# Performance work log

Measured on AMD Instinct MI355X. Metric: run time of the kernel, lower is better.

The kernel has to match this reference:

```python
import jax, jax.numpy as jnp
import numpy as np

BATCH = 16384
NUM_Q = 100000
NUM_TAGS = 1024
DIFF_FEAT = 3
DIM = 64
HIDDEN = 128


def setup_inputs() -> dict:
    key = jax.random.key(0)
    ks = jax.random.split(key, 10)
    questions = jax.random.randint(ks[0], (BATCH,), 0, NUM_Q, dtype=jnp.int64 if jax.config.jax_enable_x64 else jnp.int32)
    question_skill_targets = jax.random.randint(ks[1], (BATCH, NUM_TAGS), 0, 2, dtype=jnp.int32)
    difficulty_feats = jax.random.normal(ks[2], (BATCH, DIFF_FEAT), dtype=jnp.float32)
    Q_emb = jax.random.normal(ks[3], (NUM_Q, DIM), dtype=jnp.float32) * 0.02
    S_emb = jax.random.normal(ks[4], (NUM_TAGS, DIM), dtype=jnp.float32) * 0.02
    W_diff = jax.random.normal(ks[5], (DIFF_FEAT, DIM), dtype=jnp.float32) * 0.1
    b_diff = jnp.zeros((DIM,), dtype=jnp.float32)
    W_fc = jax.random.normal(ks[6], (3 * DIM + 3, HIDDEN), dtype=jnp.float32) * 0.05
    b_fc = jnp.zeros((HIDDEN,), dtype=jnp.float32)
    W_out = jax.random.normal(ks[7], (HIDDEN, 1), dtype=jnp.float32) * 0.05
    b_out = jnp.zeros((1,), dtype=jnp.float32)
    return {"questions": questions, "question_skill_targets": question_skill_targets,
            "difficulty_feats": difficulty_feats, "Q_emb": Q_emb, "S_emb": S_emb,
            "W_diff": W_diff, "b_diff": b_diff, "W_fc": W_fc, "b_fc": b_fc,
            "W_out": W_out, "b_out": b_out}


def reference(questions, question_skill_targets, difficulty_feats,
              Q_emb, S_emb, W_diff, b_diff, W_fc, b_fc, W_out, b_out):
    # Ragged segment-mean over skill sets: mean of skill embeddings whose
    # multi-hot entry is nonzero == (T @ S) / count per row.
    t = question_skill_targets.astype(jnp.float32)            # [B, T]
    counts = jnp.sum(t, axis=1, keepdims=True)                # [B, 1] (>=1 w.h.p.)
    mu_skill = (t @ S_emb) / counts                           # [B, D]
    q = Q_emb[questions]                                      # [B, D]
    a = difficulty_feats @ W_diff + b_diff                    # [B, D]
    # PNN product layer: pairwise inner products + concat linear signals
    p12 = jnp.sum(q * mu_skill, axis=-1, keepdims=True)
    p13 = jnp.sum(q * a, axis=-1, keepdims=True)
    p23 = jnp.sum(mu_skill * a, axis=-1, keepdims=True)
    z = jnp.concatenate([q, mu_skill, a, p12, p13, p23], axis=-1)  # [B, 3D+3]
    e = jax.nn.relu(z @ W_fc + b_fc)                          # [B, H]
    p = jax.nn.sigmoid(e @ W_out + b_out)[:, 0]               # [B]
    return (e, p)
```

## Files before the change

kernel.cpp:

```cpp
#include <hip/hip_runtime.h>
#include <hip/hip_bf16.h>

#define BATCH   16384
#define NTAGS   1024
#define DIM     64
#define HID     128

typedef __attribute__((ext_vector_type(8))) short bf16x8;
typedef __attribute__((ext_vector_type(4))) float f32x4;

__device__ __forceinline__ unsigned short f2bf(float v) {
    unsigned u = __builtin_bit_cast(unsigned, v);
    return (unsigned short)((u + 0x7FFFu + ((u >> 16) & 1u)) >> 16);
}
__device__ __forceinline__ float bf2f(unsigned short u) {
    return __builtin_bit_cast(float, ((unsigned)u) << 16);
}

__global__ __launch_bounds__(256) void prep_pack(const float* __restrict__ S,
                                                 const float* __restrict__ Wfc,
                                                 unsigned short* __restrict__ Spack,
                                                 unsigned short* __restrict__ Wp)
{
    int tid = blockIdx.x * 256 + threadIdx.x;
    if (tid < 65536) {
        int j = tid & 7, l = (tid >> 3) & 63, nf = (tid >> 9) & 3, ks = tid >> 11;
        int k = ks * 32 + (l >> 4) * 8 + j;
        int d = nf * 16 + (l & 15);
        Spack[tid] = f2bf(S[k * 64 + d]);
    } else if (tid < 65536 + 24576) {
        int t2 = tid - 65536;
        int j = t2 & 7, l = (t2 >> 3) & 63, ct = (t2 >> 9) & 7, kt = t2 >> 12;
        int k = kt * 32 + (l >> 4) * 8 + j;
        int col = ct * 16 + (l & 15);
        Wp[t2] = f2bf(Wfc[k * 128 + col]);
    }
}

__global__ __launch_bounds__(256) void mega_kernel(
    const int* __restrict__ questions, const int* __restrict__ T,
    const float* __restrict__ dfeat, const float* __restrict__ Qemb,
    const float* __restrict__ Wdiff, const float* __restrict__ bdiff,
    const float* __restrict__ Wfc, const float* __restrict__ bfc,
    const float* __restrict__ Wout, const float* __restrict__ bout,
    const unsigned short* __restrict__ Spack, const unsigned short* __restrict__ Wp,
    float* __restrict__ out_e, float* __restrict__ out_p)
{
    __shared__ alignas(16) unsigned short zb[4][16][200];
    __shared__ float cnt16[4][16];
    __shared__ float scal[4][16][3];

    const int tid  = threadIdx.x;
    const int lane = tid & 63;
    const int wid  = tid >> 6;
    const int g    = lane >> 4;
    const int rl   = lane & 15;
    const int wrow = (blockIdx.x * 4 + wid) * 16;

    unsigned short (*z)[200] = zb[wid];
    float* cw = cnt16[wid];
    float (*sc)[3] = scal[wid];

    f32x4 a0{}, a1{}, a2{}, a3{};
    int c = 0;
    {
        const int* tp = T + (size_t)(wrow + rl) * 1024 + g * 8;
        const unsigned short* sp = Spack + lane * 8;

        int4 t0 = *(const int4*)(tp);
        int4 t1 = *(const int4*)(tp + 4);
#pragma unroll
        for (int st = 0; st < 32; ++st) {
            int4 c0 = t0, c1 = t1;
            if (st < 31) {
                t0 = *(const int4*)(tp + (st + 1) * 32);
                t1 = *(const int4*)(tp + (st + 1) * 32 + 4);
            }
            c += c0.x + c0.y + c0.z + c0.w + c1.x + c1.y + c1.z + c1.w;
            bf16x8 af;
            af[0] = (short)((-c0.x) & 0x3F80);
            af[1] = (short)((-c0.y) & 0x3F80);
            af[2] = (short)((-c0.z) & 0x3F80);
            af[3] = (short)((-c0.w) & 0x3F80);
            af[4] = (short)((-c1.x) & 0x3F80);
            af[5] = (short)((-c1.y) & 0x3F80);
            af[6] = (short)((-c1.z) & 0x3F80);
            af[7] = (short)((-c1.w) & 0x3F80);

            const unsigned short* s2 = sp + st * 2048;
            bf16x8 b0 = *(const bf16x8*)(s2);
            bf16x8 b1 = *(const bf16x8*)(s2 + 512);
            bf16x8 b2 = *(const bf16x8*)(s2 + 1024);
            bf16x8 b3 = *(const bf16x8*)(s2 + 1536);

            a0 = __builtin_amdgcn_mfma_f32_16x16x32_bf16(af, b0, a0, 0, 0, 0);
            a1 = __builtin_amdgcn_mfma_f32_16x16x32_bf16(af, b1, a1, 0, 0, 0);
            a2 = __builtin_amdgcn_mfma_f32_16x16x32_bf16(af, b2, a2, 0, 0, 0);
            a3 = __builtin_amdgcn_mfma_f32_16x16x32_bf16(af, b3, a3, 0, 0, 0);
        }
    }
    c += __shfl_xor(c, 16);
    c += __shfl_xor(c, 32);
    if (lane < 16) cw[lane] = (float)c;

    {
        float inv[4];
#pragma unroll
        for (int r = 0; r < 4; ++r) inv[r] = 1.f / cw[g * 4 + r];
#pragma unroll
        for (int r = 0; r < 4; ++r) {
            int row = g * 4 + r;
            z[row][64 + rl]      = f2bf(a0[r] * inv[r]);
            z[row][64 + 16 + rl] = f2bf(a1[r] * inv[r]);
            z[row][64 + 32 + rl] = f2bf(a2[r] * inv[r]);
            z[row][64 + 48 + rl] = f2bf(a3[r] * inv[r]);
        }
    }

    {
        int r = lane >> 2, q4 = lane & 3, d0 = q4 * 16;
        int row = wrow + r;
        int qi = questions[row];

        float q[16], aa[16], mu[16];
#pragma unroll
        for (int b = 0; b < 4; ++b) {
            float4 v = *(const float4*)(Qemb + (size_t)qi * 64 + d0 + b * 4);
            q[b * 4 + 0] = v.x; q[b * 4 + 1] = v.y; q[b * 4 + 2] = v.z; q[b * 4 + 3] = v.w;
        }
        float f0 = dfeat[row * 3 + 0];
        float f1 = dfeat[row * 3 + 1];
        float f2 = dfeat[row * 3 + 2];
#pragma unroll
        for (int b = 0; b < 4; ++b) {
            float4 w0 = *(const float4*)(Wdiff + d0 + b * 4);
            float4 w1 = *(const float4*)(Wdiff + 64 + d0 + b * 4);
            float4 w2 = *(const float4*)(Wdiff + 128 + d0 + b * 4);
            float4 bd = *(const float4*)(bdiff + d0 + b * 4);
            aa[b * 4 + 0] = bd.x + f0 * w0.x + f1 * w1.x + f2 * w2.x;
            aa[b * 4 + 1] = bd.y + f0 * w0.y + f1 * w1.y + f2 * w2.y;
            aa[b * 4 + 2] = bd.z + f0 * w0.z + f1 * w1.z + f2 * w2.z;
            aa[b * 4 + 3] = bd.w + f0 * w0.w + f1 * w1.w + f2 * w2.w;
        }
#pragma unroll
        for (int b = 0; b < 2; ++b) {
            ushort4 m0 = *(const ushort4*)&z[r][64 + d0 + b * 8];
            ushort4 m1 = *(const ushort4*)&z[r][64 + d0 + b * 8 + 4];
            mu[b * 8 + 0] = bf2f(m0.x); mu[b * 8 + 1] = bf2f(m0.y);
            mu[b * 8 + 2] = bf2f(m0.z); mu[b * 8 + 3] = bf2f(m0.w);
            mu[b * 8 + 4] = bf2f(m1.x); mu[b * 8 + 5] = bf2f(m1.y);
            mu[b * 8 + 6] = bf2f(m1.z); mu[b * 8 + 7] = bf2f(m1.w);
        }
        float s12 = 0.f, s13 = 0.f, s23 = 0.f;
#pragma unroll
        for (int d = 0; d < 16; ++d) {
            s12 += q[d] * mu[d];
            s13 += q[d] * aa[d];
            s23 += mu[d] * aa[d];
        }
        s12 += __shfl_xor(s12, 1); s12 += __shfl_xor(s12, 2);
        s13 += __shfl_xor(s13, 1); s13 += __shfl_xor(s13, 2);
        s23 += __shfl_xor(s23, 1); s23 += __shfl_xor(s23, 2);
        if (q4 == 0) { sc[r][0] = s12; sc[r][1] = s13; sc[r][2] = s23; }

        ushort4 v;
#pragma unroll
        for (int b = 0; b < 4; ++b) {
            v.x = f2bf(q[b * 4 + 0]); v.y = f2bf(q[b * 4 + 1]);
            v.z = f2bf(q[b * 4 + 2]); v.w = f2bf(q[b * 4 + 3]);
            *(ushort4*)&z[r][d0 + b * 4] = v;
        }
#pragma unroll
        for (int b = 0; b < 4; ++b) {
            v.x = f2bf(aa[b * 4 + 0]); v.y = f2bf(aa[b * 4 + 1]);
            v.z = f2bf(aa[b * 4 + 2]); v.w = f2bf(aa[b * 4 + 3]);
            *(ushort4*)&z[r][128 + d0 + b * 4] = v;
        }
    }

    {
        bf16x8 afr[6];
#pragma unroll
        for (int kt = 0; kt < 6; ++kt)
            afr[kt] = *(const bf16x8*)&z[rl][kt * 32 + g * 8];

        float s0 = sc[g * 4 + 0][0], s1 = sc[g * 4 + 0][1], s2 = sc[g * 4 + 0][2];
        float t0_ = sc[g * 4 + 1][0], t1_ = sc[g * 4 + 1][1], t2_ = sc[g * 4 + 1][2];
        float u0 = sc[g * 4 + 2][0], u1 = sc[g * 4 + 2][1], u2 = sc[g * 4 + 2][2];
        float v0 = sc[g * 4 + 3][0], v1 = sc[g * 4 + 3][1], v2 = sc[g * 4 + 3][2];

        float pr0 = 0.f, pr1 = 0.f, pr2 = 0.f, pr3 = 0.f;
#pragma unroll
        for (int ct = 0; ct < 8; ++ct) {
            f32x4 e{};
            const unsigned short* wp = Wp + (size_t)ct * 512 + lane * 8;
#pragma unroll
            for (int kt = 0; kt < 6; ++kt) {
                bf16x8 bfr = *(const bf16x8*)(wp + (size_t)kt * 4096);
                e = __builtin_amdgcn_mfma_f32_16x16x32_bf16(afr[kt], bfr, e, 0, 0, 0);
            }
            int h = ct * 16 + rl;
            float w192 = Wfc[192 * 128 + h];
            float w193 = Wfc[193 * 128 + h];
            float w194 = Wfc[194 * 128 + h];
            float bb = bfc[h];
            float wo = Wout[h];

            float ev;
            ev = e[0] + bb + s0 * w192 + s1 * w193 + s2 * w194;
            ev = ev > 0.f ? ev : 0.f;
            out_e[(size_t)(wrow + g * 4 + 0) * 128 + h] = ev;  pr0 += ev * wo;
            ev = e[1] + bb + t0_ * w192 + t1_ * w193 + t2_ * w194;
            ev = ev > 0.f ? ev : 0.f;
            out_e[(size_t)(wrow + g * 4 + 1) * 128 + h] = ev;  pr1 += ev * wo;
            ev = e[2] + bb + u0 * w192 + u1 * w193 + u2 * w194;
            ev = ev > 0.f ? ev : 0.f;
            out_e[(size_t)(wrow + g * 4 + 2) * 128 + h] = ev;  pr2 += ev * wo;
            ev = e[3] + bb + v0 * w192 + v1 * w193 + v2 * w194;
            ev = ev > 0.f ? ev : 0.f;
            out_e[(size_t)(wrow + g * 4 + 3) * 128 + h] = ev;  pr3 += ev * wo;
        }
#pragma unroll
        for (int off = 1; off < 16; off <<= 1) {
            pr0 += __shfl_xor(pr0, off);
            pr1 += __shfl_xor(pr1, off);
            pr2 += __shfl_xor(pr2, off);
            pr3 += __shfl_xor(pr3, off);
        }
        if (rl == 0) {
            float bo = bout[0];
            out_p[wrow + g * 4 + 0] = 1.f / (1.f + expf(-(pr0 + bo)));
            out_p[wrow + g * 4 + 1] = 1.f / (1.f + expf(-(pr1 + bo)));
            out_p[wrow + g * 4 + 2] = 1.f / (1.f + expf(-(pr2 + bo)));
            out_p[wrow + g * 4 + 3] = 1.f / (1.f + expf(-(pr3 + bo)));
        }
    }
}

extern "C" void kernel_launch(void* const* d_in, const int* in_sizes, int n_in,
                              void* d_out, int out_size, void* d_ws, size_t ws_size,
                              hipStream_t stream)
{
    const int*   questions = (const int*)d_in[0];
    const int*   T         = (const int*)d_in[1];
    const float* dfeat     = (const float*)d_in[2];
    const float* Qemb      = (const float*)d_in[3];
    const float* Semb      = (const float*)d_in[4];
    const float* Wdiff     = (const float*)d_in[5];
    const float* bdiff     = (const float*)d_in[6];
    const float* Wfc       = (const float*)d_in[7];
    const float* bfc       = (const float*)d_in[8];
    const float* Wout      = (const float*)d_in[9];
    const float* bout      = (const float*)d_in[10];

    char* ws = (char*)d_ws;
    unsigned short* Spack = (unsigned short*)ws;
    unsigned short* Wp    = (unsigned short*)(ws + 131072);

    float* out_e = (float*)d_out;
    float* out_p = out_e + (size_t)BATCH * HID;

    hipLaunchKernelGGL(prep_pack, dim3(352), dim3(256), 0, stream, Semb, Wfc, Spack, Wp);
    hipLaunchKernelGGL(mega_kernel, dim3(BATCH / 64), dim3(256), 0, stream,
                       questions, T, dfeat, Qemb, Wdiff, bdiff, Wfc, bfc, Wout, bout,
                       Spack, Wp, out_e, out_p);
}
```

Measured before the change: 29.12 us.

## Deepen prefetch of multi-hot rows and skill tiles in segment-mean MFMA loop

Replaces the one-step-ahead prefetch of the 0/1 target matrix with double-buffered 8-step chunks (16 int4 registers each) and a 4-deep rotating prefetch of packed skill-embedding fragments. This keeps many more global loads in flight to hide HBM latency on the dominant 64 MB target read. It also sets launch_bounds min-blocks to 1, which lets the compiler use more registers at the risk of lower occupancy. The remaining edits rename variables to avoid clashes with the macros.

```diff
diff --git a/kernel.cpp b/kernel.cpp
--- a/kernel.cpp
+++ b/kernel.cpp
@@ -15,6 +15,18 @@
 }
 __device__ __forceinline__ float bf2f(unsigned short u) {
     return __builtin_bit_cast(float, ((unsigned)u) << 16);
+}
+__device__ __forceinline__ bf16x8 mk_af(int4 u, int4 v) {
+    bf16x8 af;
+    af[0] = (short)((-u.x) & 0x3F80);
+    af[1] = (short)((-u.y) & 0x3F80);
+    af[2] = (short)((-u.z) & 0x3F80);
+    af[3] = (short)((-u.w) & 0x3F80);
+    af[4] = (short)((-v.x) & 0x3F80);
+    af[5] = (short)((-v.y) & 0x3F80);
+    af[6] = (short)((-v.z) & 0x3F80);
+    af[7] = (short)((-v.w) & 0x3F80);
+    return af;
 }
 
 __global__ __launch_bounds__(256) void prep_pack(const float* __restrict__ S,
@@ -37,7 +49,7 @@
     }
 }
 
-__global__ __launch_bounds__(256) void mega_kernel(
+__global__ __launch_bounds__(256, 1) void mega2_kernel(
     const int* __restrict__ questions, const int* __restrict__ T,
     const float* __restrict__ dfeat, const float* __restrict__ Qemb,
     const float* __restrict__ Wdiff, const float* __restrict__ bdiff,
@@ -67,37 +79,58 @@
         const int* tp = T + (size_t)(wrow + rl) * 1024 + g * 8;
         const unsigned short* sp = Spack + lane * 8;
 
-        int4 t0 = *(const int4*)(tp);
-        int4 t1 = *(const int4*)(tp + 4);
-#pragma unroll
-        for (int st = 0; st < 32; ++st) {
-            int4 c0 = t0, c1 = t1;
-            if (st < 31) {
-                t0 = *(const int4*)(tp + (st + 1) * 32);
-                t1 = *(const int4*)(tp + (st + 1) * 32 + 4);
-            }
-            c += c0.x + c0.y + c0.z + c0.w + c1.x + c1.y + c1.z + c1.w;
-            bf16x8 af;
-            af[0] = (short)((-c0.x) & 0x3F80);
-            af[1] = (short)((-c0.y) & 0x3F80);
-            af[2] = (short)((-c0.z) & 0x3F80);
-            af[3] = (short)((-c0.w) & 0x3F80);
-            af[4] = (short)((-c1.x) & 0x3F80);
-            af[5] = (short)((-c1.y) & 0x3F80);
-            af[6] = (short)((-c1.z) & 0x3F80);
-            af[7] = (short)((-c1.w) & 0x3F80);
-
-            const unsigned short* s2 = sp + st * 2048;
-            bf16x8 b0 = *(const bf16x8*)(s2);
-            bf16x8 b1 = *(const bf16x8*)(s2 + 512);
-            bf16x8 b2 = *(const bf16x8*)(s2 + 1024);
-            bf16x8 b3 = *(const bf16x8*)(s2 + 1536);
-
-            a0 = __builtin_amdgcn_mfma_f32_16x16x32_bf16(af, b0, a0, 0, 0, 0);
-            a1 = __builtin_amdgcn_mfma_f32_16x16x32_bf16(af, b1, a1, 0, 0, 0);
-            a2 = __builtin_amdgcn_mfma_f32_16x16x32_bf16(af, b2, a2, 0, 0, 0);
-            a3 = __builtin_amdgcn_mfma_f32_16x16x32_bf16(af, b3, a3, 0, 0, 0);
-        }
+        int4 tA[16], tB[16];
+        bf16x8 s0[4], s1[4], s2[4], s3[4];
+
+#define TCHUNK(buf, kb)                                                     \
+        _Pragma("unroll") for (int i = 0; i < 8; ++i) {                     \
+            buf[2*i]   = *(const int4*)(tp + ((kb) + i) * 32);              \
+            buf[2*i+1] = *(const int4*)(tp + ((kb) + i) * 32 + 4);          \
+        }
+#define TPAIR(buf, i, kn)                                                   \
+        { buf[2*(i)]   = *(const int4*)(tp + ((kn) + (i)) * 32);            \
+          buf[2*(i)+1] = *(const int4*)(tp + ((kn) + (i)) * 32 + 4); }
+#define SLOAD(buf, ks)                                                      \
+        _Pragma("unroll") for (int f = 0; f < 4; ++f)                       \
+            buf[f] = *(const bf16x8*)(sp + (size_t)(ks) * 2048 + f * 512);
+#define KBODY(tbuf, ii, sbuf, ks)                                           \
+        { bf16x8 c0 = sbuf[0], c1 = sbuf[1], c2 = sbuf[2], c3 = sbuf[3];    \
+          if ((ks) + 4 < 32) { SLOAD(sbuf, (ks) + 4); }                     \
+          int4 u = tbuf[2*(ii)], v = tbuf[2*(ii)+1];                        \
+          c += u.x+u.y+u.z+u.w+v.x+v.y+v.z+v.w;                             \
+          bf16x8 af = mk_af(u, v);                                          \
+          a0 = __builtin_amdgcn_mfma_f32_16x16x32_bf16(af, c0, a0, 0,0,0);  \
+          a1 = __builtin_amdgcn_mfma_f32_16x16x32_bf16(af, c1, a1, 0,0,0);  \
+          a2 = __builtin_amdgcn_mfma_f32_16x16x32_bf16(af, c2, a2, 0,0,0);  \
+          a3 = __builtin_amdgcn_mfma_f32_16x16x32_bf16(af, c3, a3, 0,0,0); }
+#define CHUNK8P(tbuf, kb, nbuf, kn)                                         \
+        KBODY(tbuf,0,s0,(kb)+0) TPAIR(nbuf,0,kn)                            \
+        KBODY(tbuf,1,s1,(kb)+1) TPAIR(nbuf,1,kn)                            \
+        KBODY(tbuf,2,s2,(kb)+2) TPAIR(nbuf,2,kn)                            \
+        KBODY(tbuf,3,s3,(kb)+3) TPAIR(nbuf,3,kn)                            \
+        KBODY(tbuf,4,s0,(kb)+4) TPAIR(nbuf,4,kn)                            \
+        KBODY(tbuf,5,s1,(kb)+5) TPAIR(nbuf,5,kn)                            \
+        KBODY(tbuf,6,s2,(kb)+6) TPAIR(nbuf,6,kn)                            \
+        KBODY(tbuf,7,s3,(kb)+7) TPAIR(nbuf,7,kn)
+#define CHUNK8(tbuf, kb)                                                    \
+        KBODY(tbuf,0,s0,(kb)+0) KBODY(tbuf,1,s1,(kb)+1)                     \
+        KBODY(tbuf,2,s2,(kb)+2) KBODY(tbuf,3,s3,(kb)+3)                     \
+        KBODY(tbuf,4,s0,(kb)+4) KBODY(tbuf,5,s1,(kb)+5)                     \
+        KBODY(tbuf,6,s2,(kb)+6) KBODY(tbuf,7,s3,(kb)+7)
+
+        TCHUNK(tA, 0);
+        SLOAD(s0, 0); SLOAD(s1, 1); SLOAD(s2, 2); SLOAD(s3, 3);
+        TCHUNK(tB, 8);
+        CHUNK8P(tA, 0,  tA, 16);
+        CHUNK8P(tB, 8,  tB, 24);
+        CHUNK8(tA, 16);
+        CHUNK8(tB, 24);
+#undef TCHUNK
+#undef TPAIR
+#undef SLOAD
+#undef KBODY
+#undef CHUNK8P
+#undef CHUNK8
     }
     c += __shfl_xor(c, 16);
     c += __shfl_xor(c, 32);
@@ -118,7 +151,7 @@
     }
 
     {
-        int r = lane >> 2, q4 = lane & 3, d0 = q4 * 16;
+        int r = lane >> 2, q4l = lane & 3, d0 = q4l * 16;
         int row = wrow + r;
         int qi = questions[row];
 
@@ -161,7 +194,7 @@
         s12 += __shfl_xor(s12, 1); s12 += __shfl_xor(s12, 2);
         s13 += __shfl_xor(s13, 1); s13 += __shfl_xor(s13, 2);
         s23 += __shfl_xor(s23, 1); s23 += __shfl_xor(s23, 2);
-        if (q4 == 0) { sc[r][0] = s12; sc[r][1] = s13; sc[r][2] = s23; }
+        if (q4l == 0) { sc[r][0] = s12; sc[r][1] = s13; sc[r][2] = s23; }
 
         ushort4 v;
 #pragma unroll
@@ -184,10 +217,10 @@
         for (int kt = 0; kt < 6; ++kt)
             afr[kt] = *(const bf16x8*)&z[rl][kt * 32 + g * 8];
 
-        float s0 = sc[g * 4 + 0][0], s1 = sc[g * 4 + 0][1], s2 = sc[g * 4 + 0][2];
+        float s0_ = sc[g * 4 + 0][0], s1_ = sc[g * 4 + 0][1], s2_ = sc[g * 4 + 0][2];
         float t0_ = sc[g * 4 + 1][0], t1_ = sc[g * 4 + 1][1], t2_ = sc[g * 4 + 1][2];
-        float u0 = sc[g * 4 + 2][0], u1 = sc[g * 4 + 2][1], u2 = sc[g * 4 + 2][2];
-        float v0 = sc[g * 4 + 3][0], v1 = sc[g * 4 + 3][1], v2 = sc[g * 4 + 3][2];
+        float u0_ = sc[g * 4 + 2][0], u1_ = sc[g * 4 + 2][1], u2_ = sc[g * 4 + 2][2];
+        float v0_ = sc[g * 4 + 3][0], v1_ = sc[g * 4 + 3][1], v2_ = sc[g * 4 + 3][2];
 
         float pr0 = 0.f, pr1 = 0.f, pr2 = 0.f, pr3 = 0.f;
 #pragma unroll
@@ -207,16 +240,16 @@
             float wo = Wout[h];
 
             float ev;
-            ev = e[0] + bb + s0 * w192 + s1 * w193 + s2 * w194;
+            ev = e[0] + bb + s0_ * w192 + s1_ * w193 + s2_ * w194;
             ev = ev > 0.f ? ev : 0.f;
             out_e[(size_t)(wrow + g * 4 + 0) * 128 + h] = ev;  pr0 += ev * wo;
             ev = e[1] + bb + t0_ * w192 + t1_ * w193 + t2_ * w194;
             ev = ev > 0.f ? ev : 0.f;
             out_e[(size_t)(wrow + g * 4 + 1) * 128 + h] = ev;  pr1 += ev * wo;
-            ev = e[2] + bb + u0 * w192 + u1 * w193 + u2 * w194;
+            ev = e[2] + bb + u0_ * w192 + u1_ * w193 + u2_ * w194;
             ev = ev > 0.f ? ev : 0.f;
             out_e[(size_t)(wrow + g * 4 + 2) * 128 + h] = ev;  pr2 += ev * wo;
-            ev = e[3] + bb + v0 * w192 + v1 * w193 + v2 * w194;
+            ev = e[3] + bb + v0_ * w192 + v1_ * w193 + v2_ * w194;
             ev = ev > 0.f ? ev : 0.f;
             out_e[(size_t)(wrow + g * 4 + 3) * 128 + h] = ev;  pr3 += ev * wo;
         }
@@ -261,7 +294,7 @@
     float* out_p = out_e + (size_t)BATCH * HID;
 
     hipLaunchKernelGGL(prep_pack, dim3(352), dim3(256), 0, stream, Semb, Wfc, Spack, Wp);
-    hipLaunchKernelGGL(mega_kernel, dim3(BATCH / 64), dim3(256), 0, stream,
+    hipLaunchKernelGGL(mega2_kernel, dim3(BATCH / 64), dim3(256), 0, stream,
                        questions, T, dfeat, Qemb, Wdiff, bdiff, Wfc, bfc, Wout, bout,
                        Spack, Wp, out_e, out_p);
 }
```

After: 32.33 us. 1.11x slower.
